# Kernel tuning notes

Measured on AMD Instinct MI355X. Metric: run time of the kernel, lower is better.

The kernel has to match this reference:

```python
import jax, jax.numpy as jnp
import numpy as np

B, V, NB, NJ, NEXTRA = 512, 6890, 10, 24, 9
PARENTS = np.array([-1,0,0,0,1,2,3,4,5,6,7,8,9,9,9,12,13,14,16,17,18,19,20,21], dtype=np.int32)


def setup_inputs() -> dict:
    key = jax.random.key(0)
    ks = jax.random.split(key, 11)
    betas = jax.random.normal(ks[0], (B, NB + 1), jnp.float32) * 0.1
    betas = betas.at[:, 0].set(1.0)  # col 0 is a global scale in this SMPL variant
    body_pose = jax.random.normal(ks[1], (B, 3 * (NJ - 1)), jnp.float32) * 0.2
    global_orient = jax.random.normal(ks[2], (B, 3), jnp.float32) * 0.2
    transl = jax.random.normal(ks[3], (B, 3), jnp.float32) * 0.1
    model_scale_opt = jnp.ones((1,), jnp.float32)
    smpl_v_template = jax.random.normal(ks[4], (V, 3), jnp.float32)
    smil_v_template = jax.random.normal(ks[5], (V, 3), jnp.float32)
    shapedirs = jax.random.normal(ks[6], (V, 3, NB), jnp.float32) * 0.01
    J_regressor = jax.nn.softmax(jax.random.normal(ks[7], (NJ, V), jnp.float32), axis=1)
    lbs_weights = jax.nn.softmax(jax.random.normal(ks[8], (V, NJ), jnp.float32) * 4.0, axis=1)
    J_regressor_extra = jax.nn.softmax(jax.random.normal(ks[9], (NEXTRA, V), jnp.float32), axis=1)
    parents = jnp.asarray(PARENTS)
    return dict(betas=betas, body_pose=body_pose, global_orient=global_orient,
                transl=transl, model_scale_opt=model_scale_opt,
                smpl_v_template=smpl_v_template, smil_v_template=smil_v_template,
                shapedirs=shapedirs, J_regressor=J_regressor, lbs_weights=lbs_weights,
                J_regressor_extra=J_regressor_extra, parents=parents)


def batch_rodrigues(rvecs):
    # rvecs: [N,3] axis-angle -> [N,3,3] rotation matrices
    angle = jnp.linalg.norm(rvecs + 1e-8, axis=1, keepdims=True)  # [N,1]
    axis = rvecs / angle
    c = jnp.cos(angle)[..., None]  # [N,1,1]
    s = jnp.sin(angle)[..., None]
    rx, ry, rz = axis[:, 0], axis[:, 1], axis[:, 2]
    z = jnp.zeros_like(rx)
    K = jnp.stack([z, -rz, ry, rz, z, -rx, -ry, rx, z], axis=1).reshape(-1, 3, 3)
    I = jnp.eye(3, dtype=rvecs.dtype)
    return I + s * K + (1.0 - c) * jnp.matmul(K, K)


def _smpl_forward(betas, body_pose, global_orient, transl, model_scale_opt,
                  smpl_v_template, smil_v_template, shapedirs,
                  J_regressor, lbs_weights, J_regressor_extra):
    dtype = betas.dtype
    # ---- updateShape ----
    s = model_scale_opt[0]
    v_template = smpl_v_template * s + (1.0 - s) * smil_v_template  # [V,3]
    blend_shape = jnp.einsum('bl,mkl->bmk', betas[:, 1:], shapedirs)  # [B,V,3]
    v_shaped = (v_template[None] + blend_shape) * betas[:, :1, None]  # scale col
    J_shaped = jnp.einsum('bik,ji->bjk', v_shaped, J_regressor)  # [B,NJ,3]

    # ---- updatePose ----
    full_pose = jnp.concatenate([global_orient, body_pose], axis=1)  # [B,NJ*3]
    rot_mats = batch_rodrigues(full_pose.reshape(-1, 3)).reshape(B, NJ, 3, 3)

    # relative joint locations w.r.t. parents
    rel_joints = J_shaped.at[:, 1:].add(-J_shaped[:, PARENTS[1:]])
    top = jnp.concatenate([rot_mats, rel_joints[..., None]], axis=-1)  # [B,NJ,3,4]
    bottom = jnp.broadcast_to(
        jnp.array([0.0, 0.0, 0.0, 1.0], dtype=dtype), (B, NJ, 1, 4))
    mats = jnp.concatenate([top, bottom], axis=2)  # [B,NJ,4,4]

    # sequential kinematic-chain composition over the 24-joint tree
    chain = [mats[:, 0]]
    for i in range(1, NJ):
        chain.append(jnp.matmul(chain[PARENTS[i]], mats[:, i]))
    chain = jnp.stack(chain, axis=1)  # [B,NJ,4,4]
    posed_joints = chain[:, :, :3, 3]  # [B,NJ,3]

    # relative transforms: subtract rotated rest joints
    corr = jnp.einsum('bjmn,bjn->bjm', chain[:, :, :3, :3], J_shaped)
    A = chain.at[:, :, :3, 3].add(-corr)  # [B,NJ,4,4]

    # linear blend skinning
    T = jnp.einsum('vj,bjmn->bvmn', lbs_weights, A)  # [B,V,4,4]
    verts = jnp.einsum('bvmn,bvn->bvm', T[:, :, :3, :3], v_shaped) + T[:, :, :3, 3]

    extra_joints = jnp.einsum('bik,ji->bjk', verts, J_regressor_extra)  # [B,9,3]
    joints = jnp.concatenate([posed_joints, extra_joints], axis=1)  # [B,33,3]

    t = transl[:, None, :]
    # concat verts and joints along point dim for a single output array
    return jnp.concatenate([verts + t, joints + t], axis=1)  # [B, V+33, 3]


def reference(betas, body_pose, global_orient, transl, model_scale_opt,
              smpl_v_template, smil_v_template, shapedirs,
              J_regressor, lbs_weights, J_regressor_extra, parents):
    return _smpl_forward(betas, body_pose, global_orient, transl, model_scale_opt,
                         smpl_v_template, smil_v_template, shapedirs,
                         J_regressor, lbs_weights, J_regressor_extra)
```

## Files before the change

### kernel.cpp

```cpp
#include <hip/hip_runtime.h>


#define BATCH 512
#define NV 6890
#define NBD 10
#define NJ 24
#define NEXTRA 9
#define NOUT (NV + NJ + NEXTRA)
#define VBLK ((NV + 255) / 256)
#define BPB 4
#define PCHUNK 8
#define PCLEN ((NV + PCHUNK - 1) / PCHUNK)
#define EPN 34

__constant__ int c_par[NJ] = {-1,0,0,0,1,2,3,4,5,6,7,8,9,9,9,12,13,14,16,17,18,19,20,21};
__constant__ int c_dep[NJ] = {0,1,1,1,2,2,2,3,3,3,4,4,4,4,4,5,5,5,6,6,7,7,8,8};

__global__ __launch_bounds__(256) void transpose_kernel(
    const float* __restrict__ smpl_t,
    const float* __restrict__ smil_t,
    const float* __restrict__ sdirs,
    const float* __restrict__ lbsw,
    const float* __restrict__ msc,
    float* __restrict__ vtT,
    float* __restrict__ sdT,
    float* __restrict__ lbswT)
{
    const int v = blockIdx.x * 256 + threadIdx.x;
    if (v >= NV) return;
    const float s = msc[0];
#pragma unroll
    for (int k = 0; k < 3; ++k)
        vtT[k * NV + v] = s * smpl_t[v * 3 + k] + (1.f - s) * smil_t[v * 3 + k];
    const float2* sd2 = (const float2*)(sdirs + (size_t)v * 30);
#pragma unroll
    for (int i = 0; i < 15; ++i) {
        float2 x = sd2[i];
        sdT[(2 * i) * NV + v]     = x.x;
        sdT[(2 * i + 1) * NV + v] = x.y;
    }
    const float4* w4 = (const float4*)(lbsw + (size_t)v * NJ);
#pragma unroll
    for (int i = 0; i < 6; ++i) {
        float4 x = w4[i];
        lbswT[(4 * i) * NV + v]     = x.x;
        lbswT[(4 * i + 1) * NV + v] = x.y;
        lbswT[(4 * i + 2) * NV + v] = x.z;
        lbswT[(4 * i + 3) * NV + v] = x.w;
    }
}

__global__ __launch_bounds__(256) void pre_kernel(
    const float* __restrict__ jreg,
    const float* __restrict__ jre,
    const float* __restrict__ vtT,
    const float* __restrict__ sdT,
    const float* __restrict__ lbswT,
    float* __restrict__ jtjs_part,
    float* __restrict__ epre)
{
    const int j = blockIdx.y;

    __shared__ float red[4][EPN];
    const int lane = threadIdx.x & 63, wv = threadIdx.x >> 6;

    if (blockIdx.x < PCHUNK) {
        const int c = blockIdx.x;
        const int vbeg = c * PCLEN;
        const int vend_ = (vbeg + PCLEN < NV) ? vbeg + PCLEN : NV;

        float acc[33];
#pragma unroll
        for (int i = 0; i < 33; ++i) acc[i] = 0.f;

        for (int v = vbeg + threadIdx.x; v < vend_; v += 256) {
            const float w = jreg[j * NV + v];
#pragma unroll
            for (int k = 0; k < 3; ++k) acc[k] = fmaf(w, vtT[k * NV + v], acc[k]);
#pragma unroll
            for (int i = 0; i < 30; ++i) acc[3 + i] = fmaf(w, sdT[i * NV + v], acc[3 + i]);
        }

#pragma unroll
        for (int i = 0; i < 33; ++i) {
            float x = acc[i];
            for (int off = 32; off; off >>= 1) x += __shfl_xor(x, off, 64);
            acc[i] = x;
        }
        if (lane == 0) {
#pragma unroll
            for (int i = 0; i < 33; ++i) red[wv][i] = acc[i];
        }
        __syncthreads();
        if (threadIdx.x < 33) {
            jtjs_part[(c * NJ + j) * 33 + threadIdx.x] =
                red[0][threadIdx.x] + red[1][threadIdx.x]
              + red[2][threadIdx.x] + red[3][threadIdx.x];
        }
    } else {
        const int e = blockIdx.x - PCHUNK;

        float acc[EPN];
#pragma unroll
        for (int i = 0; i < EPN; ++i) acc[i] = 0.f;

        for (int v = threadIdx.x; v < NV; v += 256) {
            const float u = jre[e * NV + v] * lbswT[j * NV + v];
            acc[33] += u;
#pragma unroll
            for (int k = 0; k < 3; ++k) acc[k] = fmaf(u, vtT[k * NV + v], acc[k]);
#pragma unroll
            for (int i = 0; i < 30; ++i) acc[3 + i] = fmaf(u, sdT[i * NV + v], acc[3 + i]);
        }

#pragma unroll
        for (int i = 0; i < EPN; ++i) {
            float x = acc[i];
            for (int off = 32; off; off >>= 1) x += __shfl_xor(x, off, 64);
            acc[i] = x;
        }
        if (lane == 0) {
#pragma unroll
            for (int i = 0; i < EPN; ++i) red[wv][i] = acc[i];
        }
        __syncthreads();
        if (threadIdx.x < EPN) {
            epre[(e * NJ + j) * EPN + threadIdx.x] =
                red[0][threadIdx.x] + red[1][threadIdx.x]
              + red[2][threadIdx.x] + red[3][threadIdx.x];
        }
    }
}

__global__ __launch_bounds__(64) void joints_kernel(
    const float* __restrict__ betas,
    const float* __restrict__ body_pose,
    const float* __restrict__ glob_or,
    const float* __restrict__ transl,
    const float* __restrict__ jtjs_part,
    const float* __restrict__ epre,
    float* __restrict__ wsA,
    float* __restrict__ out)
{
    const int b = blockIdx.x;
    const int j = threadIdx.x;

    __shared__ float sJ[NJ][3];
    __shared__ float mats[NJ][12];
    __shared__ float chain[NJ][12];
    __shared__ float sbeta[NBD + 1];
    __shared__ float sS[NEXTRA][NJ][3];
    __shared__ float sW[NEXTRA][NJ];

    if (threadIdx.x < NBD + 1) sbeta[threadIdx.x] = betas[b * (NBD + 1) + threadIdx.x];
    __syncthreads();

    if (j < NJ) {
        float jt[33];
#pragma unroll
        for (int i = 0; i < 33; ++i) jt[i] = 0.f;
        for (int c = 0; c < PCHUNK; ++c) {
#pragma unroll
            for (int i = 0; i < 33; ++i) jt[i] += jtjs_part[(c * NJ + j) * 33 + i];
        }

        const float beta0 = sbeta[0];
#pragma unroll
        for (int k = 0; k < 3; ++k) {
            float a = jt[k];
#pragma unroll
            for (int l = 0; l < NBD; ++l) a = fmaf(sbeta[1 + l], jt[3 + k * 10 + l], a);
            sJ[j][k] = a * beta0;
        }
        float rx, ry, rz;
        if (j == 0) {
            rx = glob_or[b * 3 + 0]; ry = glob_or[b * 3 + 1]; rz = glob_or[b * 3 + 2];
        } else {
            rx = body_pose[b * 69 + (j - 1) * 3 + 0];
            ry = body_pose[b * 69 + (j - 1) * 3 + 1];
            rz = body_pose[b * 69 + (j - 1) * 3 + 2];
        }
        float ex = rx + 1e-8f, ey = ry + 1e-8f, ez = rz + 1e-8f;
        float ang = sqrtf(ex * ex + ey * ey + ez * ez);
        float inv = 1.f / ang;
        float ax = rx * inv, ay = ry * inv, az = rz * inv;
        float c = cosf(ang), s = sinf(ang), t = 1.f - c;
        mats[j][0]  = 1.f + t * (-(ay * ay + az * az));
        mats[j][1]  = -s * az + t * (ax * ay);
        mats[j][2]  =  s * ay + t * (ax * az);
        mats[j][4]  =  s * az + t * (ax * ay);
        mats[j][5]  = 1.f + t * (-(ax * ax + az * az));
        mats[j][6]  = -s * ax + t * (ay * az);
        mats[j][8]  = -s * ay + t * (ax * az);
        mats[j][9]  =  s * ax + t * (ay * az);
        mats[j][10] = 1.f + t * (-(ax * ax + ay * ay));
    }
    __syncthreads();
    if (j < NJ) {
        const int p = c_par[j];
        float t0 = sJ[j][0], t1 = sJ[j][1], t2 = sJ[j][2];
        if (p >= 0) { t0 -= sJ[p][0]; t1 -= sJ[p][1]; t2 -= sJ[p][2]; }
        mats[j][3] = t0; mats[j][7] = t1; mats[j][11] = t2;
    }
    __syncthreads();
    if (j == 0) {
#pragma unroll
        for (int k = 0; k < 12; ++k) chain[0][k] = mats[0][k];
    }
    __syncthreads();
    for (int lev = 1; lev <= 8; ++lev) {
        if (j < NJ && c_dep[j] == lev) {
            const int p = c_par[j];
            float r_[12];
#pragma unroll
            for (int r = 0; r < 3; ++r) {
#pragma unroll
                for (int col = 0; col < 4; ++col) {
                    float acc = (col == 3) ? chain[p][r * 4 + 3] : 0.f;
#pragma unroll
                    for (int q = 0; q < 3; ++q) acc = fmaf(chain[p][r * 4 + q], mats[j][q * 4 + col], acc);
                    r_[r * 4 + col] = acc;
                }
            }
#pragma unroll
            for (int k = 0; k < 12; ++k) chain[j][k] = r_[k];
        }
        __syncthreads();
    }
    if (j < NJ) {
        float A[12];
#pragma unroll
        for (int k = 0; k < 12; ++k) A[k] = chain[j][k];
        const float c0 = A[3], c1 = A[7], c2 = A[11];
        const float j0 = sJ[j][0], j1 = sJ[j][1], j2 = sJ[j][2];
        A[3]  = c0 - (A[0] * j0 + A[1] * j1 + A[2]  * j2);
        A[7]  = c1 - (A[4] * j0 + A[5] * j1 + A[6]  * j2);
        A[11] = c2 - (A[8] * j0 + A[9] * j1 + A[10] * j2);
#pragma unroll
        for (int k = 0; k < 12; ++k) wsA[((size_t)b * NJ + j) * 12 + k] = A[k];
#pragma unroll
        for (int k = 0; k < 12; ++k) mats[j][k] = A[k];
        const float tx = transl[b * 3 + 0], ty = transl[b * 3 + 1], tz = transl[b * 3 + 2];
        const size_t o = ((size_t)b * NOUT + NV + j) * 3;
        out[o + 0] = c0 + tx; out[o + 1] = c1 + ty; out[o + 2] = c2 + tz;
    }

    for (int p = threadIdx.x; p < NEXTRA * NJ; p += 64) {
        const int e  = p / NJ;
        const int jj = p - e * NJ;
        const float* ep = epre + p * EPN;
#pragma unroll
        for (int cc = 0; cc < 3; ++cc) {
            float a = ep[cc];
#pragma unroll
            for (int l = 0; l < NBD; ++l) a = fmaf(sbeta[1 + l], ep[3 + cc * 10 + l], a);
            sS[e][jj][cc] = a * sbeta[0];
        }
        sW[e][jj] = ep[33];
    }
    __syncthreads();
    if (threadIdx.x < 3 * NEXTRA) {
        const int e = threadIdx.x / 3;
        const int k = threadIdx.x - e * 3;
        float acc = 0.f;
#pragma unroll 4
        for (int jj = 0; jj < NJ; ++jj) {
            acc = fmaf(mats[jj][k * 4 + 0], sS[e][jj][0], acc);
            acc = fmaf(mats[jj][k * 4 + 1], sS[e][jj][1], acc);
            acc = fmaf(mats[jj][k * 4 + 2], sS[e][jj][2], acc);
            acc = fmaf(mats[jj][k * 4 + 3], sW[e][jj],    acc);
        }
        out[((size_t)b * NOUT + NV + NJ) * 3 + threadIdx.x] = acc + transl[b * 3 + k];
    }
}

__global__ __launch_bounds__(256) void lbs_kernel(
    const float* __restrict__ betas,
    const float* __restrict__ transl,
    const float* __restrict__ msc,
    const float* __restrict__ smpl_t,
    const float* __restrict__ smil_t,
    const float* __restrict__ sdirs,
    const float* __restrict__ lbsw,
    const float* __restrict__ wsA,
    float* __restrict__ out)
{
    const int rot = __builtin_amdgcn_readfirstlane((int)(threadIdx.x >> 6) + (int)blockIdx.x);

    const int v = blockIdx.x * 256 + threadIdx.x;
    const bool valid = v < NV;
    const int vc = valid ? v : NV - 1;
    const int b0 = blockIdx.y * BPB;
    const float s = msc[0];

    float vt[3];
#pragma unroll
    for (int k = 0; k < 3; ++k)
        vt[k] = s * smpl_t[vc * 3 + k] + (1.f - s) * smil_t[vc * 3 + k];

    float sd[30];
    {
        const float2* sd2 = (const float2*)(sdirs + (size_t)vc * 30);
#pragma unroll
        for (int i = 0; i < 15; ++i) { float2 x = sd2[i]; sd[2 * i] = x.x; sd[2 * i + 1] = x.y; }
    }
    float w[NJ];
    {
        const float4* w4 = (const float4*)(lbsw + (size_t)vc * NJ);
#pragma unroll
        for (int i = 0; i < 6; ++i) {
            float4 x = w4[i];
            w[4 * i] = x.x; w[4 * i + 1] = x.y; w[4 * i + 2] = x.z; w[4 * i + 3] = x.w;
        }
    }

#pragma unroll
    for (int bb = 0; bb < BPB; ++bb) {
        const int b = b0 + ((bb + rot) & (BPB - 1));
        const float* __restrict__ Bb = betas + b * (NBD + 1);
        const float* __restrict__ Ab = wsA + (size_t)b * NJ * 12;

        float vs[3];
#pragma unroll
        for (int k = 0; k < 3; ++k) {
            float a = vt[k];
#pragma unroll
            for (int l = 0; l < NBD; ++l) a = fmaf(Bb[1 + l], sd[k * 10 + l], a);
            vs[k] = a * Bb[0];
        }

        float T[12];
#pragma unroll
        for (int k = 0; k < 12; ++k) T[k] = 0.f;
#pragma unroll 4
        for (int jj = 0; jj < NJ; ++jj) {
            const float ww = w[jj];
#pragma unroll
            for (int k = 0; k < 12; ++k) T[k] = fmaf(ww, Ab[jj * 12 + k], T[k]);
        }

        if (valid) {
            const float tx = transl[b * 3 + 0], ty = transl[b * 3 + 1], tz = transl[b * 3 + 2];
            const size_t o = ((size_t)b * NOUT + v) * 3;
            out[o + 0] = fmaf(T[0], vs[0], fmaf(T[1], vs[1], fmaf(T[2],  vs[2], T[3])))  + tx;
            out[o + 1] = fmaf(T[4], vs[0], fmaf(T[5], vs[1], fmaf(T[6],  vs[2], T[7])))  + ty;
            out[o + 2] = fmaf(T[8], vs[0], fmaf(T[9], vs[1], fmaf(T[10], vs[2], T[11]))) + tz;
        }
    }
}

extern "C" void kernel_launch(void* const* d_in, const int* in_sizes, int n_in,
                              void* d_out, int out_size, void* d_ws, size_t ws_size,
                              hipStream_t stream) {
    const float* betas     = (const float*)d_in[0];
    const float* body_pose = (const float*)d_in[1];
    const float* glob_or   = (const float*)d_in[2];
    const float* transl    = (const float*)d_in[3];
    const float* msc       = (const float*)d_in[4];
    const float* smpl_t    = (const float*)d_in[5];
    const float* smil_t    = (const float*)d_in[6];
    const float* sdirs     = (const float*)d_in[7];
    const float* jreg      = (const float*)d_in[8];
    const float* lbsw      = (const float*)d_in[9];
    const float* jre       = (const float*)d_in[10];

    float* out  = (float*)d_out;
    float* ws   = (float*)d_ws;
    float* wsA       = ws;
    float* jtjs_part = wsA + (size_t)BATCH * NJ * 12;
    float* epre      = jtjs_part + PCHUNK * NJ * 33;
    float* vtT       = epre + NEXTRA * NJ * EPN;
    float* sdT       = vtT + 3 * NV;
    float* lbswT     = sdT + 30 * NV;

    transpose_kernel<<<VBLK, 256, 0, stream>>>(smpl_t, smil_t, sdirs, lbsw, msc,
                                               vtT, sdT, lbswT);

    dim3 gA(PCHUNK + NEXTRA, NJ);
    pre_kernel<<<gA, 256, 0, stream>>>(jreg, jre, vtT, sdT, lbswT,
                                       jtjs_part, epre);

    joints_kernel<<<BATCH, 64, 0, stream>>>(betas, body_pose, glob_or, transl,
                                            jtjs_part, epre, wsA, out);

    dim3 gC(VBLK, BATCH / BPB);
    lbs_kernel<<<gC, 256, 0, stream>>>(betas, transl, msc, smpl_t, smil_t, sdirs, lbsw, wsA, out);
}
```

Baseline: 174.6 us.

## Fuse transpose, pre-reduction and joints kernels into one persistent kernel with grid barriers

Merges three small launches (the transpose, the per-joint regressor reductions and the per-batch kinematic chain) into one 512-block kernel separated by software grid barriers built on atomic counters, plus a memset to reset the counters. The aim is to remove launch gaps and tail idling between tiny dependent kernels. The joints stage now runs with 256 threads per block instead of 64, and correctness depends on all 512 blocks being resident at once, otherwise the barriers deadlock.

```diff
diff --git a/kernel.cpp b/kernel.cpp
--- a/kernel.cpp
+++ b/kernel.cpp
@@ -12,139 +12,50 @@
 #define PCHUNK 8
 #define PCLEN ((NV + PCHUNK - 1) / PCHUNK)
 #define EPN 34
+#define PREB ((PCHUNK + NEXTRA) * NJ)
+#define GRIDB 512
 
 __constant__ int c_par[NJ] = {-1,0,0,0,1,2,3,4,5,6,7,8,9,9,9,12,13,14,16,17,18,19,20,21};
 __constant__ int c_dep[NJ] = {0,1,1,1,2,2,2,3,3,3,4,4,4,4,4,5,5,5,6,6,7,7,8,8};
 
-__global__ __launch_bounds__(256) void transpose_kernel(
+__device__ __forceinline__ void grid_barrier(int* cnt)
+{
+    __syncthreads();
+    if (threadIdx.x == 0) {
+        __threadfence();
+        __hip_atomic_fetch_add(cnt, 1, __ATOMIC_ACQ_REL, __HIP_MEMORY_SCOPE_AGENT);
+        while (__hip_atomic_load(cnt, __ATOMIC_ACQUIRE, __HIP_MEMORY_SCOPE_AGENT) < GRIDB)
+            __builtin_amdgcn_s_sleep(2);
+    }
+    __syncthreads();
+    __threadfence();
+}
+
+__global__ __launch_bounds__(256) void fused_kernel(
+    const float* __restrict__ jreg,
+    const float* __restrict__ jre,
+    const float* __restrict__ lbsw,
     const float* __restrict__ smpl_t,
     const float* __restrict__ smil_t,
     const float* __restrict__ sdirs,
-    const float* __restrict__ lbsw,
     const float* __restrict__ msc,
-    float* __restrict__ vtT,
-    float* __restrict__ sdT,
-    float* __restrict__ lbswT)
-{
-    const int v = blockIdx.x * 256 + threadIdx.x;
-    if (v >= NV) return;
-    const float s = msc[0];
-#pragma unroll
-    for (int k = 0; k < 3; ++k)
-        vtT[k * NV + v] = s * smpl_t[v * 3 + k] + (1.f - s) * smil_t[v * 3 + k];
-    const float2* sd2 = (const float2*)(sdirs + (size_t)v * 30);
-#pragma unroll
-    for (int i = 0; i < 15; ++i) {
-        float2 x = sd2[i];
-        sdT[(2 * i) * NV + v]     = x.x;
-        sdT[(2 * i + 1) * NV + v] = x.y;
-    }
-    const float4* w4 = (const float4*)(lbsw + (size_t)v * NJ);
-#pragma unroll
-    for (int i = 0; i < 6; ++i) {
-        float4 x = w4[i];
-        lbswT[(4 * i) * NV + v]     = x.x;
-        lbswT[(4 * i + 1) * NV + v] = x.y;
-        lbswT[(4 * i + 2) * NV + v] = x.z;
-        lbswT[(4 * i + 3) * NV + v] = x.w;
-    }
-}
-
-__global__ __launch_bounds__(256) void pre_kernel(
-    const float* __restrict__ jreg,
-    const float* __restrict__ jre,
-    const float* __restrict__ vtT,
-    const float* __restrict__ sdT,
-    const float* __restrict__ lbswT,
-    float* __restrict__ jtjs_part,
-    float* __restrict__ epre)
-{
-    const int j = blockIdx.y;
-
-    __shared__ float red[4][EPN];
-    const int lane = threadIdx.x & 63, wv = threadIdx.x >> 6;
-
-    if (blockIdx.x < PCHUNK) {
-        const int c = blockIdx.x;
-        const int vbeg = c * PCLEN;
-        const int vend_ = (vbeg + PCLEN < NV) ? vbeg + PCLEN : NV;
-
-        float acc[33];
-#pragma unroll
-        for (int i = 0; i < 33; ++i) acc[i] = 0.f;
-
-        for (int v = vbeg + threadIdx.x; v < vend_; v += 256) {
-            const float w = jreg[j * NV + v];
-#pragma unroll
-            for (int k = 0; k < 3; ++k) acc[k] = fmaf(w, vtT[k * NV + v], acc[k]);
-#pragma unroll
-            for (int i = 0; i < 30; ++i) acc[3 + i] = fmaf(w, sdT[i * NV + v], acc[3 + i]);
-        }
-
-#pragma unroll
-        for (int i = 0; i < 33; ++i) {
-            float x = acc[i];
-            for (int off = 32; off; off >>= 1) x += __shfl_xor(x, off, 64);
-            acc[i] = x;
-        }
-        if (lane == 0) {
-#pragma unroll
-            for (int i = 0; i < 33; ++i) red[wv][i] = acc[i];
-        }
-        __syncthreads();
-        if (threadIdx.x < 33) {
-            jtjs_part[(c * NJ + j) * 33 + threadIdx.x] =
-                red[0][threadIdx.x] + red[1][threadIdx.x]
-              + red[2][threadIdx.x] + red[3][threadIdx.x];
-        }
-    } else {
-        const int e = blockIdx.x - PCHUNK;
-
-        float acc[EPN];
-#pragma unroll
-        for (int i = 0; i < EPN; ++i) acc[i] = 0.f;
-
-        for (int v = threadIdx.x; v < NV; v += 256) {
-            const float u = jre[e * NV + v] * lbswT[j * NV + v];
-            acc[33] += u;
-#pragma unroll
-            for (int k = 0; k < 3; ++k) acc[k] = fmaf(u, vtT[k * NV + v], acc[k]);
-#pragma unroll
-            for (int i = 0; i < 30; ++i) acc[3 + i] = fmaf(u, sdT[i * NV + v], acc[3 + i]);
-        }
-
-#pragma unroll
-        for (int i = 0; i < EPN; ++i) {
-            float x = acc[i];
-            for (int off = 32; off; off >>= 1) x += __shfl_xor(x, off, 64);
-            acc[i] = x;
-        }
-        if (lane == 0) {
-#pragma unroll
-            for (int i = 0; i < EPN; ++i) red[wv][i] = acc[i];
-        }
-        __syncthreads();
-        if (threadIdx.x < EPN) {
-            epre[(e * NJ + j) * EPN + threadIdx.x] =
-                red[0][threadIdx.x] + red[1][threadIdx.x]
-              + red[2][threadIdx.x] + red[3][threadIdx.x];
-        }
-    }
-}
-
-__global__ __launch_bounds__(64) void joints_kernel(
     const float* __restrict__ betas,
     const float* __restrict__ body_pose,
     const float* __restrict__ glob_or,
     const float* __restrict__ transl,
-    const float* __restrict__ jtjs_part,
-    const float* __restrict__ epre,
+    float* __restrict__ vtT,
+    float* __restrict__ sdT,
+    float* __restrict__ lbswT,
+    float* __restrict__ jtjs_part,
+    float* __restrict__ epre,
     float* __restrict__ wsA,
-    float* __restrict__ out)
+    float* __restrict__ out,
+    int* __restrict__ bar)
 {
-    const int b = blockIdx.x;
-    const int j = threadIdx.x;
-
+    const int bid = blockIdx.x;
+    const int tid = threadIdx.x;
+
+    __shared__ float red[4][EPN];
     __shared__ float sJ[NJ][3];
     __shared__ float mats[NJ][12];
     __shared__ float chain[NJ][12];
@@ -152,125 +63,229 @@
     __shared__ float sS[NEXTRA][NJ][3];
     __shared__ float sW[NEXTRA][NJ];
 
-    if (threadIdx.x < NBD + 1) sbeta[threadIdx.x] = betas[b * (NBD + 1) + threadIdx.x];
-    __syncthreads();
-
-    if (j < NJ) {
-        float jt[33];
-#pragma unroll
-        for (int i = 0; i < 33; ++i) jt[i] = 0.f;
-        for (int c = 0; c < PCHUNK; ++c) {
-#pragma unroll
-            for (int i = 0; i < 33; ++i) jt[i] += jtjs_part[(c * NJ + j) * 33 + i];
-        }
-
-        const float beta0 = sbeta[0];
-#pragma unroll
-        for (int k = 0; k < 3; ++k) {
-            float a = jt[k];
-#pragma unroll
-            for (int l = 0; l < NBD; ++l) a = fmaf(sbeta[1 + l], jt[3 + k * 10 + l], a);
-            sJ[j][k] = a * beta0;
-        }
-        float rx, ry, rz;
+    if (bid < VBLK) {
+        const int v = bid * 256 + tid;
+        if (v < NV) {
+            const float s = msc[0];
+#pragma unroll
+            for (int k = 0; k < 3; ++k)
+                vtT[k * NV + v] = s * smpl_t[v * 3 + k] + (1.f - s) * smil_t[v * 3 + k];
+            const float2* sd2 = (const float2*)(sdirs + (size_t)v * 30);
+#pragma unroll
+            for (int i = 0; i < 15; ++i) {
+                float2 x = sd2[i];
+                sdT[(2 * i) * NV + v]     = x.x;
+                sdT[(2 * i + 1) * NV + v] = x.y;
+            }
+            const float4* w4 = (const float4*)(lbsw + (size_t)v * NJ);
+#pragma unroll
+            for (int i = 0; i < 6; ++i) {
+                float4 x = w4[i];
+                lbswT[(4 * i) * NV + v]     = x.x;
+                lbswT[(4 * i + 1) * NV + v] = x.y;
+                lbswT[(4 * i + 2) * NV + v] = x.z;
+                lbswT[(4 * i + 3) * NV + v] = x.w;
+            }
+        }
+    }
+    grid_barrier(&bar[0]);
+
+    if (bid < PREB) {
+        const int x = bid % (PCHUNK + NEXTRA);
+        const int j = bid / (PCHUNK + NEXTRA);
+        const int lane = tid & 63, wv = tid >> 6;
+
+        if (x < PCHUNK) {
+            const int c = x;
+            const int vbeg = c * PCLEN;
+            const int vend_ = (vbeg + PCLEN < NV) ? vbeg + PCLEN : NV;
+
+            float acc[33];
+#pragma unroll
+            for (int i = 0; i < 33; ++i) acc[i] = 0.f;
+
+            for (int v = vbeg + tid; v < vend_; v += 256) {
+                const float w = jreg[j * NV + v];
+#pragma unroll
+                for (int k = 0; k < 3; ++k) acc[k] = fmaf(w, vtT[k * NV + v], acc[k]);
+#pragma unroll
+                for (int i = 0; i < 30; ++i) acc[3 + i] = fmaf(w, sdT[i * NV + v], acc[3 + i]);
+            }
+
+#pragma unroll
+            for (int i = 0; i < 33; ++i) {
+                float xx = acc[i];
+                for (int off = 32; off; off >>= 1) xx += __shfl_xor(xx, off, 64);
+                acc[i] = xx;
+            }
+            if (lane == 0) {
+#pragma unroll
+                for (int i = 0; i < 33; ++i) red[wv][i] = acc[i];
+            }
+            __syncthreads();
+            if (tid < 33) {
+                jtjs_part[(c * NJ + j) * 33 + tid] =
+                    red[0][tid] + red[1][tid] + red[2][tid] + red[3][tid];
+            }
+        } else {
+            const int e = x - PCHUNK;
+
+            float acc[EPN];
+#pragma unroll
+            for (int i = 0; i < EPN; ++i) acc[i] = 0.f;
+
+            for (int v = tid; v < NV; v += 256) {
+                const float u = jre[e * NV + v] * lbswT[j * NV + v];
+                acc[33] += u;
+#pragma unroll
+                for (int k = 0; k < 3; ++k) acc[k] = fmaf(u, vtT[k * NV + v], acc[k]);
+#pragma unroll
+                for (int i = 0; i < 30; ++i) acc[3 + i] = fmaf(u, sdT[i * NV + v], acc[3 + i]);
+            }
+
+#pragma unroll
+            for (int i = 0; i < EPN; ++i) {
+                float xx = acc[i];
+                for (int off = 32; off; off >>= 1) xx += __shfl_xor(xx, off, 64);
+                acc[i] = xx;
+            }
+            if (lane == 0) {
+#pragma unroll
+                for (int i = 0; i < EPN; ++i) red[wv][i] = acc[i];
+            }
+            __syncthreads();
+            if (tid < EPN) {
+                epre[(e * NJ + j) * EPN + tid] =
+                    red[0][tid] + red[1][tid] + red[2][tid] + red[3][tid];
+            }
+        }
+    }
+    grid_barrier(&bar[1]);
+
+    {
+        const int b = bid;
+        const int j = tid;
+
+        if (tid < NBD + 1) sbeta[tid] = betas[b * (NBD + 1) + tid];
+        __syncthreads();
+
+        if (j < NJ) {
+            float jt[33];
+#pragma unroll
+            for (int i = 0; i < 33; ++i) jt[i] = 0.f;
+            for (int c = 0; c < PCHUNK; ++c) {
+#pragma unroll
+                for (int i = 0; i < 33; ++i) jt[i] += jtjs_part[(c * NJ + j) * 33 + i];
+            }
+
+            const float beta0 = sbeta[0];
+#pragma unroll
+            for (int k = 0; k < 3; ++k) {
+                float a = jt[k];
+#pragma unroll
+                for (int l = 0; l < NBD; ++l) a = fmaf(sbeta[1 + l], jt[3 + k * 10 + l], a);
+                sJ[j][k] = a * beta0;
+            }
+            float rx, ry, rz;
+            if (j == 0) {
+                rx = glob_or[b * 3 + 0]; ry = glob_or[b * 3 + 1]; rz = glob_or[b * 3 + 2];
+            } else {
+                rx = body_pose[b * 69 + (j - 1) * 3 + 0];
+                ry = body_pose[b * 69 + (j - 1) * 3 + 1];
+                rz = body_pose[b * 69 + (j - 1) * 3 + 2];
+            }
+            float ex = rx + 1e-8f, ey = ry + 1e-8f, ez = rz + 1e-8f;
+            float ang = sqrtf(ex * ex + ey * ey + ez * ez);
+            float inv = 1.f / ang;
+            float ax = rx * inv, ay = ry * inv, az = rz * inv;
+            float c = cosf(ang), s = sinf(ang), t = 1.f - c;
+            mats[j][0]  = 1.f + t * (-(ay * ay + az * az));
+            mats[j][1]  = -s * az + t * (ax * ay);
+            mats[j][2]  =  s * ay + t * (ax * az);
+            mats[j][4]  =  s * az + t * (ax * ay);
+            mats[j][5]  = 1.f + t * (-(ax * ax + az * az));
+            mats[j][6]  = -s * ax + t * (ay * az);
+            mats[j][8]  = -s * ay + t * (ax * az);
+            mats[j][9]  =  s * ax + t * (ay * az);
+            mats[j][10] = 1.f + t * (-(ax * ax + ay * ay));
+        }
+        __syncthreads();
+        if (j < NJ) {
+            const int p = c_par[j];
+            float t0 = sJ[j][0], t1 = sJ[j][1], t2 = sJ[j][2];
+            if (p >= 0) { t0 -= sJ[p][0]; t1 -= sJ[p][1]; t2 -= sJ[p][2]; }
+            mats[j][3] = t0; mats[j][7] = t1; mats[j][11] = t2;
+        }
+        __syncthreads();
         if (j == 0) {
-            rx = glob_or[b * 3 + 0]; ry = glob_or[b * 3 + 1]; rz = glob_or[b * 3 + 2];
-        } else {
-            rx = body_pose[b * 69 + (j - 1) * 3 + 0];
-            ry = body_pose[b * 69 + (j - 1) * 3 + 1];
-            rz = body_pose[b * 69 + (j - 1) * 3 + 2];
-        }
-        float ex = rx + 1e-8f, ey = ry + 1e-8f, ez = rz + 1e-8f;
-        float ang = sqrtf(ex * ex + ey * ey + ez * ez);
-        float inv = 1.f / ang;
-        float ax = rx * inv, ay = ry * inv, az = rz * inv;
-        float c = cosf(ang), s = sinf(ang), t = 1.f - c;
-        mats[j][0]  = 1.f + t * (-(ay * ay + az * az));
-        mats[j][1]  = -s * az + t * (ax * ay);
-        mats[j][2]  =  s * ay + t * (ax * az);
-        mats[j][4]  =  s * az + t * (ax * ay);
-        mats[j][5]  = 1.f + t * (-(ax * ax + az * az));
-        mats[j][6]  = -s * ax + t * (ay * az);
-        mats[j][8]  = -s * ay + t * (ax * az);
-        mats[j][9]  =  s * ax + t * (ay * az);
-        mats[j][10] = 1.f + t * (-(ax * ax + ay * ay));
-    }
-    __syncthreads();
-    if (j < NJ) {
-        const int p = c_par[j];
-        float t0 = sJ[j][0], t1 = sJ[j][1], t2 = sJ[j][2];
-        if (p >= 0) { t0 -= sJ[p][0]; t1 -= sJ[p][1]; t2 -= sJ[p][2]; }
-        mats[j][3] = t0; mats[j][7] = t1; mats[j][11] = t2;
-    }
-    __syncthreads();
-    if (j == 0) {
-#pragma unroll
-        for (int k = 0; k < 12; ++k) chain[0][k] = mats[0][k];
-    }
-    __syncthreads();
-    for (int lev = 1; lev <= 8; ++lev) {
-        if (j < NJ && c_dep[j] == lev) {
-            const int p = c_par[j];
-            float r_[12];
-#pragma unroll
-            for (int r = 0; r < 3; ++r) {
-#pragma unroll
-                for (int col = 0; col < 4; ++col) {
-                    float acc = (col == 3) ? chain[p][r * 4 + 3] : 0.f;
-#pragma unroll
-                    for (int q = 0; q < 3; ++q) acc = fmaf(chain[p][r * 4 + q], mats[j][q * 4 + col], acc);
-                    r_[r * 4 + col] = acc;
+#pragma unroll
+            for (int k = 0; k < 12; ++k) chain[0][k] = mats[0][k];
+        }
+        __syncthreads();
+        for (int lev = 1; lev <= 8; ++lev) {
+            if (j < NJ && c_dep[j] == lev) {
+                const int p = c_par[j];
+                float r_[12];
+#pragma unroll
+                for (int r = 0; r < 3; ++r) {
+#pragma unroll
+                    for (int col = 0; col < 4; ++col) {
+                        float acc = (col == 3) ? chain[p][r * 4 + 3] : 0.f;
+#pragma unroll
+                        for (int q = 0; q < 3; ++q) acc = fmaf(chain[p][r * 4 + q], mats[j][q * 4 + col], acc);
+                        r_[r * 4 + col] = acc;
+                    }
                 }
-            }
-#pragma unroll
-            for (int k = 0; k < 12; ++k) chain[j][k] = r_[k];
+#pragma unroll
+                for (int k = 0; k < 12; ++k) chain[j][k] = r_[k];
+            }
+            __syncthreads();
+        }
+        if (j < NJ) {
+            float A[12];
+#pragma unroll
+            for (int k = 0; k < 12; ++k) A[k] = chain[j][k];
+            const float c0 = A[3], c1 = A[7], c2 = A[11];
+            const float j0 = sJ[j][0], j1 = sJ[j][1], j2 = sJ[j][2];
+            A[3]  = c0 - (A[0] * j0 + A[1] * j1 + A[2]  * j2);
+            A[7]  = c1 - (A[4] * j0 + A[5] * j1 + A[6]  * j2);
+            A[11] = c2 - (A[8] * j0 + A[9] * j1 + A[10] * j2);
+#pragma unroll
+            for (int k = 0; k < 12; ++k) wsA[((size_t)b * NJ + j) * 12 + k] = A[k];
+#pragma unroll
+            for (int k = 0; k < 12; ++k) mats[j][k] = A[k];
+            const float tx = transl[b * 3 + 0], ty = transl[b * 3 + 1], tz = transl[b * 3 + 2];
+            const size_t o = ((size_t)b * NOUT + NV + j) * 3;
+            out[o + 0] = c0 + tx; out[o + 1] = c1 + ty; out[o + 2] = c2 + tz;
+        }
+
+        for (int p = tid; p < NEXTRA * NJ; p += 256) {
+            const int e  = p / NJ;
+            const int jj = p - e * NJ;
+            const float* ep = epre + p * EPN;
+#pragma unroll
+            for (int cc = 0; cc < 3; ++cc) {
+                float a = ep[cc];
+#pragma unroll
+                for (int l = 0; l < NBD; ++l) a = fmaf(sbeta[1 + l], ep[3 + cc * 10 + l], a);
+                sS[e][jj][cc] = a * sbeta[0];
+            }
+            sW[e][jj] = ep[33];
         }
         __syncthreads();
-    }
-    if (j < NJ) {
-        float A[12];
-#pragma unroll
-        for (int k = 0; k < 12; ++k) A[k] = chain[j][k];
-        const float c0 = A[3], c1 = A[7], c2 = A[11];
-        const float j0 = sJ[j][0], j1 = sJ[j][1], j2 = sJ[j][2];
-        A[3]  = c0 - (A[0] * j0 + A[1] * j1 + A[2]  * j2);
-        A[7]  = c1 - (A[4] * j0 + A[5] * j1 + A[6]  * j2);
-        A[11] = c2 - (A[8] * j0 + A[9] * j1 + A[10] * j2);
-#pragma unroll
-        for (int k = 0; k < 12; ++k) wsA[((size_t)b * NJ + j) * 12 + k] = A[k];
-#pragma unroll
-        for (int k = 0; k < 12; ++k) mats[j][k] = A[k];
-        const float tx = transl[b * 3 + 0], ty = transl[b * 3 + 1], tz = transl[b * 3 + 2];
-        const size_t o = ((size_t)b * NOUT + NV + j) * 3;
-        out[o + 0] = c0 + tx; out[o + 1] = c1 + ty; out[o + 2] = c2 + tz;
-    }
-
-    for (int p = threadIdx.x; p < NEXTRA * NJ; p += 64) {
-        const int e  = p / NJ;
-        const int jj = p - e * NJ;
-        const float* ep = epre + p * EPN;
-#pragma unroll
-        for (int cc = 0; cc < 3; ++cc) {
-            float a = ep[cc];
-#pragma unroll
-            for (int l = 0; l < NBD; ++l) a = fmaf(sbeta[1 + l], ep[3 + cc * 10 + l], a);
-            sS[e][jj][cc] = a * sbeta[0];
-        }
-        sW[e][jj] = ep[33];
-    }
-    __syncthreads();
-    if (threadIdx.x < 3 * NEXTRA) {
-        const int e = threadIdx.x / 3;
-        const int k = threadIdx.x - e * 3;
-        float acc = 0.f;
+        if (tid < 3 * NEXTRA) {
+            const int e = tid / 3;
+            const int k = tid - e * 3;
+            float acc = 0.f;
 #pragma unroll 4
-        for (int jj = 0; jj < NJ; ++jj) {
-            acc = fmaf(mats[jj][k * 4 + 0], sS[e][jj][0], acc);
-            acc = fmaf(mats[jj][k * 4 + 1], sS[e][jj][1], acc);
-            acc = fmaf(mats[jj][k * 4 + 2], sS[e][jj][2], acc);
-            acc = fmaf(mats[jj][k * 4 + 3], sW[e][jj],    acc);
-        }
-        out[((size_t)b * NOUT + NV + NJ) * 3 + threadIdx.x] = acc + transl[b * 3 + k];
+            for (int jj = 0; jj < NJ; ++jj) {
+                acc = fmaf(mats[jj][k * 4 + 0], sS[e][jj][0], acc);
+                acc = fmaf(mats[jj][k * 4 + 1], sS[e][jj][1], acc);
+                acc = fmaf(mats[jj][k * 4 + 2], sS[e][jj][2], acc);
+                acc = fmaf(mats[jj][k * 4 + 3], sW[e][jj],    acc);
+            }
+            out[((size_t)b * NOUT + NV + NJ) * 3 + tid] = acc + transl[b * 3 + k];
+        }
     }
 }
 
@@ -372,16 +387,14 @@
     float* vtT       = epre + NEXTRA * NJ * EPN;
     float* sdT       = vtT + 3 * NV;
     float* lbswT     = sdT + 30 * NV;
-
-    transpose_kernel<<<VBLK, 256, 0, stream>>>(smpl_t, smil_t, sdirs, lbsw, msc,
-                                               vtT, sdT, lbswT);
-
-    dim3 gA(PCHUNK + NEXTRA, NJ);
-    pre_kernel<<<gA, 256, 0, stream>>>(jreg, jre, vtT, sdT, lbswT,
-                                       jtjs_part, epre);
-
-    joints_kernel<<<BATCH, 64, 0, stream>>>(betas, body_pose, glob_or, transl,
-                                            jtjs_part, epre, wsA, out);
+    int*   bar       = (int*)(lbswT + 24 * NV);
+
+    hipMemsetAsync(bar, 0, 2 * sizeof(int), stream);
+
+    fused_kernel<<<GRIDB, 256, 0, stream>>>(
+        jreg, jre, lbsw, smpl_t, smil_t, sdirs, msc,
+        betas, body_pose, glob_or, transl,
+        vtT, sdT, lbswT, jtjs_part, epre, wsA, out, bar);
 
     dim3 gC(VBLK, BATCH / BPB);
     lbs_kernel<<<gC, 256, 0, stream>>>(betas, transl, msc, smpl_t, smil_t, sdirs, lbsw, wsA, out);
```

New measurement: 575.4 us. 229% more time.
